# Performance work log

Measured on AMD Instinct MI355X. Metric: run time of the kernel, lower is better.

## Reference

```python
import jax, jax.numpy as jnp
import numpy as np


def _glorot(key, shape):
    fan_in, fan_out = shape[0], shape[1]
    lim = np.sqrt(6.0 / (fan_in + fan_out))
    return jax.random.uniform(key, shape, jnp.float32, -lim, lim)


def setup_inputs() -> dict:
    key = jax.random.key(0)
    ks = jax.random.split(key, 32)
    B, NR, NT = 16384, 64, 128
    inp = {
        "tier0_features": jax.random.normal(ks[0], (B, 44), jnp.float32),
        "robot_features": jax.random.normal(ks[1], (B, NR, 6), jnp.float32),
        "track_features": jax.random.normal(ks[2], (B, NT, 7), jnp.float32),
        # robot SetEncoder: 6 -> 64 -> 64 -> 32
        "rw1": _glorot(ks[3], (6, 64)),  "rb1": jnp.zeros((64,), jnp.float32),
        "rw2": _glorot(ks[4], (64, 64)), "rb2": jnp.zeros((64,), jnp.float32),
        "rw3": _glorot(ks[5], (64, 32)), "rb3": jnp.zeros((32,), jnp.float32),
        # track SetEncoder: 7 -> 64 -> 64 -> 32
        "tw1": _glorot(ks[6], (7, 64)),  "tb1": jnp.zeros((64,), jnp.float32),
        "tw2": _glorot(ks[7], (64, 64)), "tb2": jnp.zeros((64,), jnp.float32),
        "tw3": _glorot(ks[8], (64, 32)), "tb3": jnp.zeros((32,), jnp.float32),
        # head MLP: 108 -> 128 -> 128 -> 64 -> 1
        "mw1": _glorot(ks[9], (108, 128)),  "mb1": jnp.zeros((128,), jnp.float32),
        "mw2": _glorot(ks[10], (128, 128)), "mb2": jnp.zeros((128,), jnp.float32),
        "mw3": _glorot(ks[11], (128, 64)),  "mb3": jnp.zeros((64,), jnp.float32),
        "mw4": _glorot(ks[12], (64, 1)),    "mb4": jnp.zeros((1,), jnp.float32),
    }
    return inp


def _set_encode(x, w1, b1, w2, b2, w3, b3):
    # x: [B, N, d_in] -> pooled [B, 32]; mask=None path: mean+max over set dim
    h = jax.nn.relu(jnp.einsum('bnd,dh->bnh', x, w1) + b1)
    h = jax.nn.relu(jnp.einsum('bnh,hk->bnk', h, w2) + b2)
    e = jnp.einsum('bnk,ko->bno', h, w3) + b3
    return (e.mean(axis=1) + e.max(axis=1)) * 0.5


def reference(tier0_features, robot_features, track_features,
              rw1, rb1, rw2, rb2, rw3, rb3,
              tw1, tb1, tw2, tb2, tw3, tb3,
              mw1, mb1, mw2, mb2, mw3, mb3, mw4, mb4):
    robot_emb = _set_encode(robot_features, rw1, rb1, rw2, rb2, rw3, rb3)  # [B,32]
    track_emb = _set_encode(track_features, tw1, tb1, tw2, tb2, tw3, tb3)  # [B,32]
    c = jnp.concatenate([tier0_features, robot_emb, track_emb], axis=1)    # [B,108]
    h = jax.nn.relu(c @ mw1 + mb1)
    h = jax.nn.relu(h @ mw2 + mb2)
    h = jax.nn.relu(h @ mw3 + mb3)
    return (h @ mw4 + mb4).squeeze(-1)  # [B]
```

## Files before the change

### kernel.cpp

```cpp
#include <hip/hip_runtime.h>
#include <hip/hip_bf16.h>

#define DEV_INLINE __device__ __forceinline__

typedef __bf16 bf16x8 __attribute__((ext_vector_type(8)));
typedef float  floatx4 __attribute__((ext_vector_type(4)));

DEV_INLINE bf16x8 ld_frag(const __bf16* p) {
    union { uint4 u; bf16x8 v; } t;
    t.u = *(const uint4*)p;
    return t.v;
}
DEV_INLINE bf16x8 pack_relu2(floatx4 a, floatx4 b) {
    float2 p0 = {fmaxf(a[0], 0.0f), fmaxf(a[1], 0.0f)};
    float2 p1 = {fmaxf(a[2], 0.0f), fmaxf(a[3], 0.0f)};
    float2 p2 = {fmaxf(b[0], 0.0f), fmaxf(b[1], 0.0f)};
    float2 p3 = {fmaxf(b[2], 0.0f), fmaxf(b[3], 0.0f)};
    union { __hip_bfloat162 h[4]; bf16x8 v; } t;
    t.h[0] = __float22bfloat162_rn(p0);
    t.h[1] = __float22bfloat162_rn(p1);
    t.h[2] = __float22bfloat162_rn(p2);
    t.h[3] = __float22bfloat162_rn(p3);
    return t.v;
}
DEV_INLINE floatx4 vmax4(floatx4 a, floatx4 b) {
    floatx4 r;
#pragma unroll
    for (int i = 0; i < 4; ++i) r[i] = fmaxf(a[i], b[i]);
    return r;
}

template<int N, int Kp, int Ks>
DEV_INLINE void tp(__bf16* dst, const float* __restrict__ src, int idx0, int stride) {
    for (int e = idx0; e < N * Kp; e += stride) {
        int n = e / Kp, k = e - n * Kp;
        dst[e] = (k < Ks) ? (__bf16)src[k * N + n] : (__bf16)0.0f;
    }
}
template<int N, int Kp, int Ks>
DEV_INLINE void tp_b(__bf16* dst, const float* __restrict__ src,
                     const float* __restrict__ bias, int idx0, int stride) {
    for (int e = idx0; e < N * Kp; e += stride) {
        int n = e / Kp, k = e - n * Kp;
        float v = (k < Ks) ? src[k * N + n] : ((k == Ks) ? bias[n] : 0.0f);
        dst[e] = (__bf16)v;
    }
}
template<int N, int K>
DEV_INLINE void tp_perm(__bf16* dst, const float* __restrict__ src, int idx0, int stride) {
    for (int e = idx0; e < N * K; e += stride) {
        int n = e / K, kh = e - n * K;
        int qd = (kh >> 3) & 3, kq = kh >> 5, j = kh & 7;
        int c = (2 * kq + (j >> 2)) * 16 + qd * 4 + (j & 3);
        dst[e] = (__bf16)src[c * N + n];
    }
}

__global__ __launch_bounds__(256)
void prep_kernel(const float* __restrict__ rw1, const float* __restrict__ rb1,
                 const float* __restrict__ rw2, const float* __restrict__ rw3,
                 const float* __restrict__ tw1, const float* __restrict__ tb1,
                 const float* __restrict__ tw2, const float* __restrict__ tw3,
                 const float* __restrict__ mw1, const float* __restrict__ mw2,
                 const float* __restrict__ mw3, __bf16* __restrict__ wb)
{
    int i0 = blockIdx.x * 256 + threadIdx.x;
    int st = gridDim.x * 256;
    tp_b   < 64,  32,   6>(wb + 0,     rw1, rb1, i0, st);
    tp_perm< 64,  64>     (wb + 2048,  rw2, i0, st);
    tp_perm< 32,  64>     (wb + 6144,  rw3, i0, st);
    tp_b   < 64,  32,   7>(wb + 8192,  tw1, tb1, i0, st);
    tp_perm< 64,  64>     (wb + 10240, tw2, i0, st);
    tp_perm< 32,  64>     (wb + 14336, tw3, i0, st);
    tp     <128, 128, 108>(wb + 16384, mw1, i0, st);
    tp_perm<128, 128>     (wb + 32768, mw2, i0, st);
    tp_perm< 64, 128>     (wb + 49152, mw3, i0, st);
}

struct __align__(16) EncSmem {
    __bf16 wt[8192];
    float2 pb[2 * 128];
    float  bs[64];
    __bf16 xs[2][128 * 8];
};

template<int DIN>
DEV_INLINE void x_load(const float* __restrict__ X, int bid, int tid, float (&g)[4]) {
    const float* src = X + (size_t)bid * 128 * DIN;
#pragma unroll
    for (int p = 0; p < 4; ++p) {
        int e = tid + p * 256;
        if ((DIN == 6) ? (p < 3) : (e < 128 * 7)) g[p] = src[e];
    }
}
template<int DIN>
DEV_INLINE void x_store(__bf16* xbuf, int tid, const float (&g)[4]) {
#pragma unroll
    for (int p = 0; p < 4; ++p) {
        int e = tid + p * 256;
        if ((DIN == 6) ? (p < 3) : (e < 128 * 7)) {
            int r = e / DIN, k = e - r * DIN;
            xbuf[r * 8 + k] = (__bf16)g[p];
        }
    }
}

template<int DIN, int S, int ITERS>
DEV_INLINE void enc_loop(EncSmem& sm, const float* __restrict__ X,
                         const __bf16* __restrict__ wsrc,
                         const float* __restrict__ b2, const float* __restrict__ b3,
                         __bf16* __restrict__ out, int bid0)
{
    constexpr int NB = 128 / S;
    const int tid = threadIdx.x;
    const int w   = tid >> 6;
    const int l64 = tid & 63;
    const int ln  = l64 & 15;
    const int qd  = l64 >> 4;

    if (tid < 64) sm.bs[tid] = b2[tid];

    for (int c = tid; c < 1024; c += 256) {
        uint4 v = *(const uint4*)(wsrc + c * 8);
        int byte = c * 16;
        int dst  = (c < 256) ? byte
                             : (byte ^ (((byte >> 7) & 7) << 4));
        *(uint4*)((char*)sm.wt + dst) = v;
    }

    {
        __bf16* xf = &sm.xs[0][0];
        if (DIN == 6) {
            union { __bf16 h[2]; uint32_t u; } c;
            c.h[0] = (__bf16)1.0f; c.h[1] = (__bf16)0.0f;
            *(uint32_t*)&xf[tid * 8 + 6] = c.u;
        } else {
            xf[tid * 8 + 7] = (__bf16)1.0f;
        }
    }
    const float b3f = (tid < NB * 32) ? b3[tid & 31] : 0.0f;

    const int wb1   = (ln * 32 + qd * 8) * 2;
    const int wb64a = ((ln * 64 + qd * 8) * 2)       ^ ((ln & 7) << 4);
    const int wb64b = ((ln * 64 + 32 + qd * 8) * 2)  ^ ((ln & 7) << 4);
    const char* wtb = (const char*)sm.wt;

    bf16x8 zf;
#pragma unroll
    for (int j = 0; j < 8; ++j) zf[j] = (__bf16)0.0f;
    const floatx4 z4 = {0.0f, 0.0f, 0.0f, 0.0f};

    float g[4];
    x_load<DIN>(X, bid0, tid, g);
    x_store<DIN>(sm.xs[0], tid, g);
    __syncthreads();

    int cur = 0, pbuf = 0;
    for (int it = 0; it < ITERS; ++it) {
        const int bid = bid0 + it;
        if (it + 1 < ITERS) x_load<DIN>(X, bid + 1, tid, g);

        bf16x8 xb[2];
#pragma unroll
        for (int t = 0; t < 2; ++t) {
            bf16x8 v = zf;
            if (qd == 0) {
                const int row = (2 * w + t) * 16 + ln;
                v = ld_frag(&sm.xs[cur][row * 8]);
            }
            xb[t] = v;
        }

        floatx4 a1[2][4];
#pragma unroll
        for (int mt = 0; mt < 4; ++mt) {
            bf16x8 wf = ld_frag((const __bf16*)(wtb + wb1 + mt * 1024));
#pragma unroll
            for (int t = 0; t < 2; ++t)
                a1[t][mt] = __builtin_amdgcn_mfma_f32_16x16x32_bf16(wf, xb[t], z4, 0, 0, 0);
        }
        bf16x8 f1[2][2];
#pragma unroll
        for (int t = 0; t < 2; ++t)
#pragma unroll
            for (int kq = 0; kq < 2; ++kq)
                f1[t][kq] = pack_relu2(a1[t][2 * kq], a1[t][2 * kq + 1]);

        bf16x8 f2[2][2];
#pragma unroll
        for (int pr = 0; pr < 2; ++pr) {
            floatx4 a2[2][2];
#pragma unroll
            for (int m = 0; m < 2; ++m) {
                const int mt = pr * 2 + m;
                floatx4 bv = *(const floatx4*)&sm.bs[mt * 16 + qd * 4];
                bf16x8 wf0 = ld_frag((const __bf16*)(wtb + 4096 + mt * 2048 + wb64a));
                bf16x8 wf1 = ld_frag((const __bf16*)(wtb + 4096 + mt * 2048 + wb64b));
#pragma unroll
                for (int t = 0; t < 2; ++t) {
                    floatx4 acc;
                    acc = __builtin_amdgcn_mfma_f32_16x16x32_bf16(wf0, f1[t][0], bv, 0, 0, 0);
                    acc = __builtin_amdgcn_mfma_f32_16x16x32_bf16(wf1, f1[t][1], acc, 0, 0, 0);
                    a2[t][m] = acc;
                }
            }
#pragma unroll
            for (int t = 0; t < 2; ++t)
                f2[t][pr] = pack_relu2(a2[t][0], a2[t][1]);
        }

        floatx4 a3[2][2];
#pragma unroll
        for (int mt = 0; mt < 2; ++mt) {
            bf16x8 wf0 = ld_frag((const __bf16*)(wtb + 12288 + mt * 2048 + wb64a));
            bf16x8 wf1 = ld_frag((const __bf16*)(wtb + 12288 + mt * 2048 + wb64b));
#pragma unroll
            for (int t = 0; t < 2; ++t) {
                floatx4 acc;
                acc = __builtin_amdgcn_mfma_f32_16x16x32_bf16(f2[t][0], wf0, z4, 0, 0, 0);
                acc = __builtin_amdgcn_mfma_f32_16x16x32_bf16(f2[t][1], wf1, acc, 0, 0, 0);
                a3[t][mt] = acc;
            }
        }

        float2 part[2];
#pragma unroll
        for (int mt = 0; mt < 2; ++mt) {
            floatx4 sv = a3[0][mt] + a3[1][mt];
            floatx4 mv = vmax4(a3[0][mt], a3[1][mt]);
            float s = (sv[0] + sv[1]) + (sv[2] + sv[3]);
            float m = fmaxf(fmaxf(mv[0], mv[1]), fmaxf(mv[2], mv[3]));
            s += __shfl_xor(s, 16); m = fmaxf(m, __shfl_xor(m, 16));
            s += __shfl_xor(s, 32); m = fmaxf(m, __shfl_xor(m, 32));
            part[mt] = make_float2(s, m);
        }

        if (it + 1 < ITERS) x_store<DIN>(sm.xs[cur ^ 1], tid, g);

        if (qd == 0) {
            sm.pb[pbuf * 128 + w * 32 + ln]      = part[0];
            sm.pb[pbuf * 128 + w * 32 + 16 + ln] = part[1];
        }
        __syncthreads();

        if (tid < NB * 32) {
            const int b = tid >> 5, f = tid & 31;
            constexpr int WPB = 4 / NB;
            float s = 0.0f, m = -3.4e38f;
#pragma unroll
            for (int wv = 0; wv < WPB; ++wv) {
                float2 v = sm.pb[pbuf * 128 + (b * WPB + wv) * 32 + f];
                s += v.x;
                m = fmaxf(m, v.y);
            }
            out[((size_t)bid * NB + b) * 32 + f] =
                (__bf16)(0.5f * (s * (1.0f / S) + m) + b3f);
        }
        cur ^= 1; pbuf ^= 1;
    }
}

__global__ __launch_bounds__(256, 6)
void enc_fused(const float* __restrict__ rX, const float* __restrict__ tX,
               const __bf16* __restrict__ wb,
               const float* __restrict__ rb2, const float* __restrict__ rb3,
               const float* __restrict__ tb2, const float* __restrict__ tb3,
               __bf16* __restrict__ remb, __bf16* __restrict__ temb)
{
    __shared__ EncSmem sm;
    if ((int)blockIdx.x < 1024)
        enc_loop<6, 64, 8>(sm, rX, wb, rb2, rb3, remb, blockIdx.x * 8);
    else
        enc_loop<7, 128, 8>(sm, tX, wb + 8192, tb2, tb3, temb,
                            ((int)blockIdx.x - 1024) * 8);
}

__global__ __launch_bounds__(256)
void head_mfma(const float* __restrict__ t0,
               const __bf16* __restrict__ remb, const __bf16* __restrict__ temb,
               const __bf16* __restrict__ hw1, const float* __restrict__ b1,
               const __bf16* __restrict__ hw2, const float* __restrict__ b2,
               const __bf16* __restrict__ hw3, const float* __restrict__ b3,
               const float* __restrict__ w4, const float* __restrict__ b4,
               float* __restrict__ out)
{
    __shared__ __align__(16) __bf16 cb[64 * 136];

    const int tid = threadIdx.x;
    const int w   = tid >> 6;
    const int l64 = tid & 63;
    const int ln  = l64 & 15;
    const int qd  = l64 >> 4;
    const int g0  = blockIdx.x * 64;

    for (int i = tid; i < 64 * 44; i += 256) {
        int r = i / 44, k = i - r * 44;
        cb[r * 136 + k] = (__bf16)t0[(size_t)(g0 + r) * 44 + k];
    }
    for (int i = tid; i < 64 * 32; i += 256) {
        int r = i >> 5, k = i & 31;
        cb[r * 136 + 44 + k] = remb[(size_t)(g0 + r) * 32 + k];
        cb[r * 136 + 76 + k] = temb[(size_t)(g0 + r) * 32 + k];
    }
    for (int i = tid; i < 64 * 20; i += 256) {
        int r = i / 20, k = i - r * 20;
        cb[r * 136 + 108 + k] = (__bf16)0.0f;
    }
    __syncthreads();

    bf16x8 cf[4];
#pragma unroll
    for (int kq = 0; kq < 4; ++kq)
        cf[kq] = ld_frag(&cb[(w * 16 + ln) * 136 + kq * 32 + qd * 8]);
    floatx4 acc1[8];
#pragma unroll
    for (int mt = 0; mt < 8; ++mt) {
        float4 bv = *(const float4*)&b1[mt * 16 + qd * 4];
        floatx4 acc = (floatx4){bv.x, bv.y, bv.z, bv.w};
#pragma unroll
        for (int kq = 0; kq < 4; ++kq) {
            bf16x8 af = ld_frag(&hw1[(mt * 16 + ln) * 128 + kq * 32 + qd * 8]);
            acc = __builtin_amdgcn_mfma_f32_16x16x32_bf16(af, cf[kq], acc, 0, 0, 0);
        }
        acc1[mt] = acc;
    }
    bf16x8 f1[4];
#pragma unroll
    for (int kq = 0; kq < 4; ++kq)
        f1[kq] = pack_relu2(acc1[2 * kq], acc1[2 * kq + 1]);

    floatx4 acc2[8];
#pragma unroll
    for (int mt = 0; mt < 8; ++mt) {
        float4 bv = *(const float4*)&b2[mt * 16 + qd * 4];
        floatx4 acc = (floatx4){bv.x, bv.y, bv.z, bv.w};
#pragma unroll
        for (int kq = 0; kq < 4; ++kq) {
            bf16x8 af = ld_frag(&hw2[(mt * 16 + ln) * 128 + kq * 32 + qd * 8]);
            acc = __builtin_amdgcn_mfma_f32_16x16x32_bf16(af, f1[kq], acc, 0, 0, 0);
        }
        acc2[mt] = acc;
    }
    bf16x8 f2[4];
#pragma unroll
    for (int kq = 0; kq < 4; ++kq)
        f2[kq] = pack_relu2(acc2[2 * kq], acc2[2 * kq + 1]);

    floatx4 acc3[4];
#pragma unroll
    for (int mt = 0; mt < 4; ++mt) {
        float4 bv = *(const float4*)&b3[mt * 16 + qd * 4];
        floatx4 acc = (floatx4){bv.x, bv.y, bv.z, bv.w};
#pragma unroll
        for (int kq = 0; kq < 4; ++kq) {
            bf16x8 af = ld_frag(&hw3[(mt * 16 + ln) * 128 + kq * 32 + qd * 8]);
            acc = __builtin_amdgcn_mfma_f32_16x16x32_bf16(af, f2[kq], acc, 0, 0, 0);
        }
        acc3[mt] = acc;
    }

    float part = 0.0f;
#pragma unroll
    for (int mt = 0; mt < 4; ++mt) {
        float4 wv = *(const float4*)&w4[mt * 16 + qd * 4];
        part = fmaf(fmaxf(acc3[mt][0], 0.0f), wv.x, part);
        part = fmaf(fmaxf(acc3[mt][1], 0.0f), wv.y, part);
        part = fmaf(fmaxf(acc3[mt][2], 0.0f), wv.z, part);
        part = fmaf(fmaxf(acc3[mt][3], 0.0f), wv.w, part);
    }
    part += __shfl_xor(part, 16);
    part += __shfl_xor(part, 32);
    if (qd == 0)
        out[g0 + w * 16 + ln] = part + b4[0];
}

extern "C" void kernel_launch(void* const* d_in, const int* in_sizes, int n_in,
                              void* d_out, int out_size, void* d_ws, size_t ws_size,
                              hipStream_t stream)
{
    const float* t0  = (const float*)d_in[0];
    const float* rX  = (const float*)d_in[1];
    const float* tX  = (const float*)d_in[2];
    const float* rw1 = (const float*)d_in[3];  const float* rb1 = (const float*)d_in[4];
    const float* rw2 = (const float*)d_in[5];  const float* rb2 = (const float*)d_in[6];
    const float* rw3 = (const float*)d_in[7];  const float* rb3 = (const float*)d_in[8];
    const float* tw1 = (const float*)d_in[9];  const float* tb1 = (const float*)d_in[10];
    const float* tw2 = (const float*)d_in[11]; const float* tb2 = (const float*)d_in[12];
    const float* tw3 = (const float*)d_in[13]; const float* tb3 = (const float*)d_in[14];
    const float* mw1 = (const float*)d_in[15]; const float* mb1 = (const float*)d_in[16];
    const float* mw2 = (const float*)d_in[17]; const float* mb2 = (const float*)d_in[18];
    const float* mw3 = (const float*)d_in[19]; const float* mb3 = (const float*)d_in[20];
    const float* mw4 = (const float*)d_in[21]; const float* mb4 = (const float*)d_in[22];
    float* out = (float*)d_out;

    const int B = 16384;
    __bf16* remb = (__bf16*)d_ws;
    __bf16* temb = (__bf16*)((char*)d_ws + ((size_t)1 << 20));
    __bf16* wb   = (__bf16*)((char*)d_ws + ((size_t)2 << 20));
    const __bf16* mw1b = wb + 16384; const __bf16* mw2b = wb + 32768;
    const __bf16* mw3b = wb + 49152;

    prep_kernel<<<64, 256, 0, stream>>>(rw1, rb1, rw2, rw3, tw1, tb1, tw2, tw3,
                                        mw1, mw2, mw3, wb);
    enc_fused<<<3072, 256, 0, stream>>>(rX, tX, wb,
                                        rb2, rb3, tb2, tb3,
                                        remb, temb);
    head_mfma<<<B / 64, 256, 0, stream>>>(t0, remb, temb,
                                          mw1b, mb1, mw2b, mb2, mw3b, mb3,
                                          mw4, mb4, out);
}
```

Measured before the change: 211.6 us.

## Keep layer-1 weights in registers, relayout LDS weights, retune grid and vectorize head loads

The first-layer weight fragments now live in registers, loaded once from global memory, so shared memory holds only the layer-2 and layer-3 weights. Those are stored in a fragment-contiguous layout that replaces the XOR-swizzled addressing. With the smaller LDS footprint, the occupancy hint goes from 6 to 8 blocks, and robot blocks process 4 batches each instead of 8, so the grid grows to 4096 blocks. ReLU is applied after bf16 packing using a packed integer max, which also maps NaN inputs differently, and the head kernel's staging loads and stores are vectorized. The extra registers for the weight fragments could pressure the tighter occupancy target.

```diff
diff --git a/kernel.cpp b/kernel.cpp
--- a/kernel.cpp
+++ b/kernel.cpp
@@ -5,6 +5,7 @@
 
 typedef __bf16 bf16x8 __attribute__((ext_vector_type(8)));
 typedef float  floatx4 __attribute__((ext_vector_type(4)));
+typedef short  shortx2 __attribute__((ext_vector_type(2)));
 
 DEV_INLINE bf16x8 ld_frag(const __bf16* p) {
     union { uint4 u; bf16x8 v; } t;
@@ -12,15 +13,14 @@
     return t.v;
 }
 DEV_INLINE bf16x8 pack_relu2(floatx4 a, floatx4 b) {
-    float2 p0 = {fmaxf(a[0], 0.0f), fmaxf(a[1], 0.0f)};
-    float2 p1 = {fmaxf(a[2], 0.0f), fmaxf(a[3], 0.0f)};
-    float2 p2 = {fmaxf(b[0], 0.0f), fmaxf(b[1], 0.0f)};
-    float2 p3 = {fmaxf(b[2], 0.0f), fmaxf(b[3], 0.0f)};
-    union { __hip_bfloat162 h[4]; bf16x8 v; } t;
-    t.h[0] = __float22bfloat162_rn(p0);
-    t.h[1] = __float22bfloat162_rn(p1);
-    t.h[2] = __float22bfloat162_rn(p2);
-    t.h[3] = __float22bfloat162_rn(p3);
+    union { __hip_bfloat162 h[4]; shortx2 s[4]; bf16x8 v; } t;
+    t.h[0] = __float22bfloat162_rn({a[0], a[1]});
+    t.h[1] = __float22bfloat162_rn({a[2], a[3]});
+    t.h[2] = __float22bfloat162_rn({b[0], b[1]});
+    t.h[3] = __float22bfloat162_rn({b[2], b[3]});
+    const shortx2 z = {0, 0};
+#pragma unroll
+    for (int i = 0; i < 4; ++i) t.s[i] = __builtin_elementwise_max(t.s[i], z);
     return t.v;
 }
 DEV_INLINE floatx4 vmax4(floatx4 a, floatx4 b) {
@@ -78,7 +78,7 @@
 }
 
 struct __align__(16) EncSmem {
-    __bf16 wt[8192];
+    __bf16 wt[6144];
     float2 pb[2 * 128];
     float  bs[64];
     __bf16 xs[2][128 * 8];
@@ -120,12 +120,13 @@
 
     if (tid < 64) sm.bs[tid] = b2[tid];
 
-    for (int c = tid; c < 1024; c += 256) {
-        uint4 v = *(const uint4*)(wsrc + c * 8);
-        int byte = c * 16;
-        int dst  = (c < 256) ? byte
-                             : (byte ^ (((byte >> 7) & 7) << 4));
-        *(uint4*)((char*)sm.wt + dst) = v;
+    for (int c = tid; c < 768; c += 256) {
+        const bool isw2 = c < 512;
+        const int cs = isw2 ? c : c - 512;
+        uint4 v = *(const uint4*)(wsrc + (isw2 ? 2048 : 6144) + cs * 8);
+        int n = cs >> 3, r = cs & 7;
+        int cd = ((n >> 4) * 2 + (r >> 2)) * 64 + (r & 3) * 16 + (n & 15);
+        *(uint4*)&sm.wt[(isw2 ? 0 : 4096) + cd * 8] = v;
     }
 
     {
@@ -140,10 +141,12 @@
     }
     const float b3f = (tid < NB * 32) ? b3[tid & 31] : 0.0f;
 
-    const int wb1   = (ln * 32 + qd * 8) * 2;
-    const int wb64a = ((ln * 64 + qd * 8) * 2)       ^ ((ln & 7) << 4);
-    const int wb64b = ((ln * 64 + 32 + qd * 8) * 2)  ^ ((ln & 7) << 4);
-    const char* wtb = (const char*)sm.wt;
+    bf16x8 w1f[4];
+#pragma unroll
+    for (int mt = 0; mt < 4; ++mt)
+        w1f[mt] = ld_frag(&wsrc[(mt * 16 + ln) * 32 + qd * 8]);
+
+    const __bf16* wl = &sm.wt[l64 * 8];
 
     bf16x8 zf;
 #pragma unroll
@@ -173,12 +176,10 @@
 
         floatx4 a1[2][4];
 #pragma unroll
-        for (int mt = 0; mt < 4; ++mt) {
-            bf16x8 wf = ld_frag((const __bf16*)(wtb + wb1 + mt * 1024));
+        for (int mt = 0; mt < 4; ++mt)
 #pragma unroll
             for (int t = 0; t < 2; ++t)
-                a1[t][mt] = __builtin_amdgcn_mfma_f32_16x16x32_bf16(wf, xb[t], z4, 0, 0, 0);
-        }
+                a1[t][mt] = __builtin_amdgcn_mfma_f32_16x16x32_bf16(w1f[mt], xb[t], z4, 0, 0, 0);
         bf16x8 f1[2][2];
 #pragma unroll
         for (int t = 0; t < 2; ++t)
@@ -194,8 +195,8 @@
             for (int m = 0; m < 2; ++m) {
                 const int mt = pr * 2 + m;
                 floatx4 bv = *(const floatx4*)&sm.bs[mt * 16 + qd * 4];
-                bf16x8 wf0 = ld_frag((const __bf16*)(wtb + 4096 + mt * 2048 + wb64a));
-                bf16x8 wf1 = ld_frag((const __bf16*)(wtb + 4096 + mt * 2048 + wb64b));
+                bf16x8 wf0 = ld_frag(&wl[(mt * 2 + 0) * 512]);
+                bf16x8 wf1 = ld_frag(&wl[(mt * 2 + 1) * 512]);
 #pragma unroll
                 for (int t = 0; t < 2; ++t) {
                     floatx4 acc;
@@ -212,8 +213,8 @@
         floatx4 a3[2][2];
 #pragma unroll
         for (int mt = 0; mt < 2; ++mt) {
-            bf16x8 wf0 = ld_frag((const __bf16*)(wtb + 12288 + mt * 2048 + wb64a));
-            bf16x8 wf1 = ld_frag((const __bf16*)(wtb + 12288 + mt * 2048 + wb64b));
+            bf16x8 wf0 = ld_frag(&wl[4096 + (mt * 2 + 0) * 512]);
+            bf16x8 wf1 = ld_frag(&wl[4096 + (mt * 2 + 1) * 512]);
 #pragma unroll
             for (int t = 0; t < 2; ++t) {
                 floatx4 acc;
@@ -260,7 +261,7 @@
     }
 }
 
-__global__ __launch_bounds__(256, 6)
+__global__ __launch_bounds__(256, 8)
 void enc_fused(const float* __restrict__ rX, const float* __restrict__ tX,
                const __bf16* __restrict__ wb,
                const float* __restrict__ rb2, const float* __restrict__ rb3,
@@ -268,11 +269,11 @@
                __bf16* __restrict__ remb, __bf16* __restrict__ temb)
 {
     __shared__ EncSmem sm;
-    if ((int)blockIdx.x < 1024)
-        enc_loop<6, 64, 8>(sm, rX, wb, rb2, rb3, remb, blockIdx.x * 8);
+    if ((int)blockIdx.x < 2048)
+        enc_loop<6, 64, 4>(sm, rX, wb, rb2, rb3, remb, blockIdx.x * 4);
     else
         enc_loop<7, 128, 8>(sm, tX, wb + 8192, tb2, tb3, temb,
-                            ((int)blockIdx.x - 1024) * 8);
+                            ((int)blockIdx.x - 2048) * 8);
 }
 
 __global__ __launch_bounds__(256)
@@ -293,18 +294,28 @@
     const int qd  = l64 >> 4;
     const int g0  = blockIdx.x * 64;
 
-    for (int i = tid; i < 64 * 44; i += 256) {
-        int r = i / 44, k = i - r * 44;
-        cb[r * 136 + k] = (__bf16)t0[(size_t)(g0 + r) * 44 + k];
-    }
-    for (int i = tid; i < 64 * 32; i += 256) {
-        int r = i >> 5, k = i & 31;
-        cb[r * 136 + 44 + k] = remb[(size_t)(g0 + r) * 32 + k];
-        cb[r * 136 + 76 + k] = temb[(size_t)(g0 + r) * 32 + k];
-    }
-    for (int i = tid; i < 64 * 20; i += 256) {
-        int r = i / 20, k = i - r * 20;
-        cb[r * 136 + 108 + k] = (__bf16)0.0f;
+    for (int i = tid; i < 64 * 11; i += 256) {
+        int r = i / 11, c = i - r * 11;
+        float4 v = *(const float4*)&t0[(size_t)(g0 + r) * 44 + c * 4];
+        union { __hip_bfloat162 h[2]; uint2 u; } t;
+        t.h[0] = __float22bfloat162_rn({v.x, v.y});
+        t.h[1] = __float22bfloat162_rn({v.z, v.w});
+        *(uint2*)&cb[r * 136 + c * 4] = t.u;
+    }
+    {
+        int r = tid >> 2, q = tid & 3;
+        uint4 a = *(const uint4*)&remb[(size_t)(g0 + r) * 32 + q * 8];
+        uint4 b = *(const uint4*)&temb[(size_t)(g0 + r) * 32 + q * 8];
+        __bf16* p = &cb[r * 136 + 44 + q * 8];
+        *(uint2*)p       = make_uint2(a.x, a.y);
+        *(uint2*)(p + 4) = make_uint2(a.z, a.w);
+        __bf16* p2 = &cb[r * 136 + 76 + q * 8];
+        *(uint2*)p2       = make_uint2(b.x, b.y);
+        *(uint2*)(p2 + 4) = make_uint2(b.z, b.w);
+    }
+    for (int i = tid; i < 64 * 5; i += 256) {
+        int r = i / 5, c = i - r * 5;
+        *(uint2*)&cb[r * 136 + 108 + c * 4] = make_uint2(0u, 0u);
     }
     __syncthreads();
 
@@ -402,7 +413,7 @@
 
     prep_kernel<<<64, 256, 0, stream>>>(rw1, rb1, rw2, rw3, tw1, tb1, tw2, tw3,
                                         mw1, mw2, mw3, wb);
-    enc_fused<<<3072, 256, 0, stream>>>(rX, tX, wb,
+    enc_fused<<<4096, 256, 0, stream>>>(rX, tX, wb,
                                         rb2, rb3, tb2, tb3,
                                         remb, temb);
     head_mfma<<<B / 64, 256, 0, stream>>>(t0, remb, temb,
```

Measured after the change: 344.1 us. +62.6%, slower.
